# Kernel tuning notes

Hardware: AMD Instinct MI355X
Metric: run time of the kernel (lower is better)

The kernel has to match this reference:

```python
import jax, jax.numpy as jnp
import numpy as np

N, E, F, HID, HEADS, G = 20000, 320000, 64, 64, 4, 64
HC = HEADS * HID  # 256
NHID, NOUT = 256, 128
INV_SQRT2 = 0.7071067811865476


def _gat(x, src, dst, W, a_s, a_d, bias):
    # GATConv (v1), eval mode (no dropout); src/dst already include self-loops (PyG default)
    H, C = a_s.shape
    h = (x @ W).reshape(-1, H, C)  # [N,H,C]
    al_s = jnp.einsum('nhc,hc->nh', h, a_s)
    al_d = jnp.einsum('nhc,hc->nh', h, a_d)
    e = jax.nn.leaky_relu(al_s[src] + al_d[dst], 0.2)  # [Etot,H]
    m = jax.ops.segment_max(e, dst, num_segments=N)
    ex = jnp.exp(e - m[dst])
    den = jax.ops.segment_sum(ex, dst, num_segments=N)
    coef = ex / den[dst]  # softmax over incoming edges per target node
    out = jax.ops.segment_sum(h[src] * coef[:, :, None], dst, num_segments=N)
    return out.reshape(-1, H * C) + bias


def _bn(h, g, b):
    # BatchNorm1d, training-mode stats (biased var), eps=1e-5
    mu = h.mean(axis=0)
    var = h.var(axis=0)
    return g * (h - mu) * jax.lax.rsqrt(var + 1e-5) + b


def _block(x, src, dst, W1, a1s, a1d, b1, g1, be1, W2, a2s, a2d, b2, g2, be2, Wr, br, Wf, bf):
    h = jax.nn.relu(_bn(_gat(x, src, dst, W1, a1s, a1d, b1), g1, be1))
    h = jax.nn.relu(_bn(_gat(h, src, dst, W2, a2s, a2d, b2), g2, be2))
    res = x @ Wr + br
    return ((h + res) * INV_SQRT2) @ Wf + bf


def setup_inputs():
    ks = iter(jax.random.split(jax.random.key(0), 64))
    def rn(shape, scale=0.05):
        return jax.random.normal(next(ks), shape, dtype=jnp.float32) * scale
    inp = {}
    inp['x'] = jax.random.normal(next(ks), (N, F), dtype=jnp.float32)
    inp['edge_index'] = jax.random.randint(next(ks), (2, E), 0, N, dtype=jnp.int32)
    inp['batch'] = jnp.sort(jax.random.randint(next(ks), (N,), 0, G, dtype=jnp.int32))
    for b, cin in enumerate([F, HID]):
        p = 'b%d_' % b
        inp[p + 'W1'] = rn((cin, HC)); inp[p + 'a1s'] = rn((HEADS, HID)); inp[p + 'a1d'] = rn((HEADS, HID))
        inp[p + 'b1'] = jnp.zeros((HC,), jnp.float32)
        inp[p + 'g1'] = jnp.ones((HC,), jnp.float32); inp[p + 'be1'] = jnp.zeros((HC,), jnp.float32)
        inp[p + 'W2'] = rn((HC, HC)); inp[p + 'a2s'] = rn((1, HC)); inp[p + 'a2d'] = rn((1, HC))
        inp[p + 'b2'] = jnp.zeros((HC,), jnp.float32)
        inp[p + 'g2'] = jnp.ones((HC,), jnp.float32); inp[p + 'be2'] = jnp.zeros((HC,), jnp.float32)
        inp[p + 'Wr'] = rn((cin, HC)); inp[p + 'br'] = jnp.zeros((HC,), jnp.float32)
        inp[p + 'Wf'] = rn((HC, HID)); inp[p + 'bf'] = jnp.zeros((HID,), jnp.float32)
    inp['Wh1'] = rn((HID, NHID)); inp['bh1'] = jnp.zeros((NHID,), jnp.float32)
    inp['Wh2'] = rn((NHID, NOUT)); inp['bh2'] = jnp.zeros((NOUT,), jnp.float32)
    return inp


def reference(x, edge_index, batch,
              b0_W1, b0_a1s, b0_a1d, b0_b1, b0_g1, b0_be1, b0_W2, b0_a2s, b0_a2d, b0_b2, b0_g2, b0_be2, b0_Wr, b0_br, b0_Wf, b0_bf,
              b1_W1, b1_a1s, b1_a1d, b1_b1, b1_g1, b1_be1, b1_W2, b1_a2s, b1_a2d, b1_b2, b1_g2, b1_be2, b1_Wr, b1_br, b1_Wf, b1_bf,
              Wh1, bh1, Wh2, bh2):
    loops = jnp.arange(N, dtype=edge_index.dtype)
    src = jnp.concatenate([edge_index[0], loops])
    dst = jnp.concatenate([edge_index[1], loops])
    x = _block(x, src, dst, b0_W1, b0_a1s, b0_a1d, b0_b1, b0_g1, b0_be1, b0_W2, b0_a2s, b0_a2d, b0_b2, b0_g2, b0_be2, b0_Wr, b0_br, b0_Wf, b0_bf)
    x = _block(x, src, dst, b1_W1, b1_a1s, b1_a1d, b1_b1, b1_g1, b1_be1, b1_W2, b1_a2s, b1_a2d, b1_b2, b1_g2, b1_be2, b1_Wr, b1_br, b1_Wf, b1_bf)
    cnt = jax.ops.segment_sum(jnp.ones((N,), x.dtype), batch, num_segments=G)
    pooled = jax.ops.segment_sum(x, batch, num_segments=G) / jnp.maximum(cnt, 1.0)[:, None]
    h = jax.nn.relu(pooled @ Wh1 + bh1)
    return h @ Wh2 + bh2
```

## Files before the change

### kernel.cpp

```cpp
#include <hip/hip_runtime.h>

#define N_NODES 20000
#define N_EDGES 320000
#define ETOT (N_EDGES + N_NODES)
#define G_GROUPS 64

typedef __attribute__((ext_vector_type(8))) short bf16x8;
typedef __attribute__((ext_vector_type(4))) float f32x4;

__device__ __forceinline__ unsigned short f2bf(float f) {
    unsigned int u = __float_as_uint(f);
    u += 0x7fffu + ((u >> 16) & 1u);
    return (unsigned short)(u >> 16);
}
__device__ __forceinline__ float bf2f(unsigned short v) {
    return __uint_as_float(((unsigned int)v) << 16);
}
__device__ __forceinline__ unsigned int pack2bf(float a, float b) {
    return (unsigned int)f2bf(a) | ((unsigned int)f2bf(b) << 16);
}


__global__ __launch_bounds__(256) void k_hist(const int* __restrict__ ei, int* __restrict__ counts) {
    int e = blockIdx.x * 256 + threadIdx.x;
    if (e >= ETOT) return;
    int dst = (e < N_EDGES) ? ei[N_EDGES + e] : (e - N_EDGES);
    atomicAdd(&counts[dst], 1);
}

__global__ __launch_bounds__(1024) void k_scan(const int* __restrict__ counts, int* __restrict__ offs,
                                               int* __restrict__ cursor) {
    __shared__ int sdata[1024];
    const int t = threadIdx.x;
    const int chunk = (N_NODES + 1023) / 1024;
    int base = t * chunk;
    int s = 0;
    for (int i = 0; i < chunk; i++) { int idx = base + i; if (idx < N_NODES) s += counts[idx]; }
    sdata[t] = s;
    __syncthreads();
    for (int off = 1; off < 1024; off <<= 1) {
        int v = (t >= off) ? sdata[t - off] : 0;
        __syncthreads();
        sdata[t] += v;
        __syncthreads();
    }
    int prefix = (t == 0) ? 0 : sdata[t - 1];
    for (int i = 0; i < chunk; i++) {
        int idx = base + i;
        if (idx < N_NODES) {
            int cv = counts[idx];
            offs[idx] = prefix;
            cursor[idx] = prefix;
            prefix += cv;
        }
    }
    if (t == 1023) offs[N_NODES] = sdata[1023];
}

__global__ __launch_bounds__(256) void k_scatter(const int* __restrict__ ei, int* __restrict__ cursor,
                                                 int* __restrict__ csr_src) {
    int e = blockIdx.x * 256 + threadIdx.x;
    if (e >= ETOT) return;
    int src = (e < N_EDGES) ? ei[e] : (e - N_EDGES);
    int dst = (e < N_EDGES) ? ei[N_EDGES + e] : (e - N_EDGES);
    int p = atomicAdd(&cursor[dst], 1);
    csr_src[p] = src;
}


__global__ __launch_bounds__(256) void k_prepB(const float* __restrict__ W, unsigned short* __restrict__ Bf,
                                               int nfrag) {
    int s = blockIdx.x * 256 + threadIdx.x;
    if (s >= nfrag) return;
    int l = s & 63;
    int nt = (s >> 6) & 15;
    int kt = s >> 10;
    int n = nt * 16 + (l & 15);
    int kb = kt * 32 + (l >> 4) * 8;
    float v[8];
    #pragma unroll
    for (int j = 0; j < 8; j++) v[j] = W[(kb + j) * 256 + n];
    uint4 q = {pack2bf(v[0], v[1]), pack2bf(v[2], v[3]), pack2bf(v[4], v[5]), pack2bf(v[6], v[7])};
    *(uint4*)(Bf + s * 8) = q;
}


__global__ __launch_bounds__(256) void k_gemm64_dual(const float* __restrict__ x,
                                                     const unsigned short* __restrict__ Bf1,
                                                     const unsigned short* __restrict__ Bfr,
                                                     const float* __restrict__ br,
                                                     const float* __restrict__ a_s, const float* __restrict__ a_d,
                                                     unsigned short* __restrict__ hbf, float* __restrict__ res,
                                                     float* __restrict__ alS, float* __restrict__ alD) {
    const int rb = blockIdx.x >> 2, cs = blockIdx.x & 3;
    const int row0 = rb * 64;
    const int nrows = min(64, N_NODES - row0);
    const int t = threadIdx.x;
    const int w = t >> 6;
    const int l = t & 63;
    const int quad = l >> 4;
    const int colLocal = l & 15;
    __shared__ unsigned short As[8 * 64 * 8];
    __shared__ float alsm[4][64], aldm[4][64];

    const int ntg = cs * 4 + w;
    bf16x8 b1f[2], brf[2];
    #pragma unroll
    for (int kt = 0; kt < 2; kt++) {
        b1f[kt] = *(const bf16x8*)(Bf1 + ((kt * 16 + ntg) * 64 + l) * 8);
        brf[kt] = *(const bf16x8*)(Bfr + ((kt * 16 + ntg) * 64 + l) * 8);
    }

    #pragma unroll
    for (int gi = 0; gi < 2; gi++) {
        int g = 2 * w + gi;
        int kt = g >> 2, mt = g & 3;
        int sm = mt * 16 + (l & 15);
        int koff = kt * 32 + (l >> 4) * 8;
        float4 v0 = {0.f, 0.f, 0.f, 0.f}, v1 = {0.f, 0.f, 0.f, 0.f};
        if (sm < nrows) {
            v0 = *(const float4*)(x + (row0 + sm) * 64 + koff);
            v1 = *(const float4*)(x + (row0 + sm) * 64 + koff + 4);
        }
        uint4 q = {pack2bf(v0.x, v0.y), pack2bf(v0.z, v0.w), pack2bf(v1.x, v1.y), pack2bf(v1.z, v1.w)};
        *(uint4*)(As + (g * 64 + l) * 8) = q;
    }
    __syncthreads();

    f32x4 acc1[4], acc2[4];
    #pragma unroll
    for (int mt = 0; mt < 4; mt++) {
        acc1[mt] = (f32x4){0.f, 0.f, 0.f, 0.f};
        acc2[mt] = (f32x4){0.f, 0.f, 0.f, 0.f};
    }
    #pragma unroll
    for (int kt = 0; kt < 2; kt++) {
        #pragma unroll
        for (int mt = 0; mt < 4; mt++) {
            bf16x8 af = *(const bf16x8*)(As + ((kt * 4 + mt) * 64 + l) * 8);
            acc1[mt] = __builtin_amdgcn_mfma_f32_16x16x32_bf16(af, b1f[kt], acc1[mt], 0, 0, 0);
            acc2[mt] = __builtin_amdgcn_mfma_f32_16x16x32_bf16(af, brf[kt], acc2[mt], 0, 0, 0);
        }
    }

    const int col = cs * 64 + w * 16 + colLocal;
    const float brv = br[col];
    const float asv = a_s[col];
    const float adv = a_d[col];
    #pragma unroll
    for (int mt = 0; mt < 4; mt++) {
        #pragma unroll
        for (int r = 0; r < 4; r++) {
            float v1 = acc1[mt][r];
            int lr = mt * 16 + quad * 4 + r;
            bool ok = lr < nrows;
            int row = row0 + lr;
            if (ok) {
                hbf[row * 256 + col] = f2bf(v1);
                res[row * 256 + col] = acc2[mt][r] + brv;
            }
            float ps = v1 * asv, pd = v1 * adv;
            #pragma unroll
            for (int off = 1; off < 16; off <<= 1) {
                ps += __shfl_xor(ps, off);
                pd += __shfl_xor(pd, off);
            }
            if (colLocal == 0) {
                alsm[w][lr] = ps;
                aldm[w][lr] = pd;
            }
        }
    }
    __syncthreads();
    if (t < 64 && t < nrows) {
        float s = (alsm[0][t] + alsm[1][t]) + (alsm[2][t] + alsm[3][t]);
        float d = (aldm[0][t] + aldm[1][t]) + (aldm[2][t] + aldm[3][t]);
        alS[(row0 + t) * 4 + cs] = s;
        alD[(row0 + t) * 4 + cs] = d;
    }
}


template <int H>
__global__ __launch_bounds__(256) void k_agg(const unsigned short* __restrict__ hbf, const float* __restrict__ alS,
                                             const float* __restrict__ alD, const int* __restrict__ offs,
                                             const int* __restrict__ csr_src, const float* __restrict__ bias,
                                             float* __restrict__ out) {
    int node = blockIdx.x * 4 + (threadIdx.x >> 6);
    int lane = threadIdx.x & 63;
    if (node >= N_NODES) return;
    const int head = (H == 4) ? (lane >> 4) : 0;
    const float ald = alD[node * H + head];
    int e0 = offs[node], e1 = offs[node + 1];
    const unsigned short* hp = hbf + lane * 4;
    float den = 0.f, a0 = 0.f, a1 = 0.f, a2 = 0.f, a3 = 0.f;
    int e = e0;
    for (; e + 8 <= e1; e += 8) {
        int s[8];
        #pragma unroll
        for (int i = 0; i < 8; i++) s[i] = csr_src[e + i];
        ushort4 hq[8];
        #pragma unroll
        for (int i = 0; i < 8; i++) hq[i] = *(const ushort4*)(hp + s[i] * 256);
        float w[8];
        #pragma unroll
        for (int i = 0; i < 8; i++) {
            float v = alS[s[i] * H + head] + ald;
            v = (v > 0.f) ? v : 0.2f * v;
            w[i] = __expf(v);
        }
        #pragma unroll
        for (int i = 0; i < 8; i++) {
            den += w[i];
            a0 += w[i] * bf2f(hq[i].x); a1 += w[i] * bf2f(hq[i].y);
            a2 += w[i] * bf2f(hq[i].z); a3 += w[i] * bf2f(hq[i].w);
        }
    }
    for (; e < e1; e++) {
        int s = csr_src[e];
        float v = alS[s * H + head] + ald;
        v = (v > 0.f) ? v : 0.2f * v;
        float w = __expf(v);
        ushort4 hq = *(const ushort4*)(hp + s * 256);
        den += w;
        a0 += w * bf2f(hq.x); a1 += w * bf2f(hq.y); a2 += w * bf2f(hq.z); a3 += w * bf2f(hq.w);
    }
    float inv = 1.f / den;
    const float4 bv = *(const float4*)(bias + lane * 4);
    float4 o = {a0 * inv + bv.x, a1 * inv + bv.y, a2 * inv + bv.z, a3 * inv + bv.w};
    *(float4*)(out + node * 256 + lane * 4) = o;
}


__global__ __launch_bounds__(256) void k_bnstats_fin(const float* __restrict__ x, float* __restrict__ sum,
                                                     float* __restrict__ sumsq, const float* __restrict__ g,
                                                     const float* __restrict__ be, float* __restrict__ scale,
                                                     float* __restrict__ shift, int* __restrict__ counter) {
    const int c = threadIdx.x;
    float s = 0.f, q = 0.f;
    for (int r = blockIdx.x; r < N_NODES; r += gridDim.x) {
        float v = x[r * 256 + c];
        s += v; q += v * v;
    }
    atomicAdd(&sum[c], s);
    atomicAdd(&sumsq[c], q);
    __threadfence();
    __syncthreads();
    __shared__ int lastFlag;
    if (c == 0) lastFlag = (atomicAdd(counter, 1) == (int)gridDim.x - 1);
    __syncthreads();
    if (lastFlag) {
        float S = atomicAdd(&sum[c], 0.f);
        float Q = atomicAdd(&sumsq[c], 0.f);
        float mu = S * (1.f / N_NODES);
        float var = Q * (1.f / N_NODES) - mu * mu;
        float sc = g[c] * rsqrtf(var + 1e-5f);
        scale[c] = sc;
        shift[c] = be[c] - mu * sc;
        sum[c] = 0.f;
        sumsq[c] = 0.f;
        if (c == 0) *counter = 0;
    }
}


__global__ __launch_bounds__(256) void k_gemm256_mfma(const float* __restrict__ A, const float* __restrict__ scale,
                                                      const float* __restrict__ shift,
                                                      const unsigned short* __restrict__ Bf,
                                                      const float* __restrict__ a_s, const float* __restrict__ a_d,
                                                      unsigned short* __restrict__ C, float* __restrict__ alSp,
                                                      float* __restrict__ alDp) {
    const int rb = blockIdx.x >> 2, cs = blockIdx.x & 3;
    const int row0 = rb * 64;
    const int nrows = min(64, N_NODES - row0);
    const int t = threadIdx.x;
    const int w = t >> 6;
    const int l = t & 63;
    const int quad = l >> 4;
    const int colLocal = l & 15;
    __shared__ unsigned short As[2 * 4 * 64 * 8];
    __shared__ float scs[256], shs[256];
    scs[t] = scale[t];
    shs[t] = shift[t];

    const int ntg = cs * 4 + w;
    bf16x8 bfrag[8];
    #pragma unroll
    for (int kt = 0; kt < 8; kt++)
        bfrag[kt] = *(const bf16x8*)(Bf + ((kt * 16 + ntg) * 64 + l) * 8);

    f32x4 acc[4];
    #pragma unroll
    for (int mt = 0; mt < 4; mt++) acc[mt] = (f32x4){0.f, 0.f, 0.f, 0.f};

    const int smt = (t >> 6) & 3;
    const int sm = smt * 16 + (l & 15);
    const int skoff = (l >> 4) * 8;

    for (int kc = 0; kc < 4; kc++) {
        __syncthreads();
        #pragma unroll
        for (int kt2 = 0; kt2 < 2; kt2++) {
            int k = kc * 64 + kt2 * 32 + skoff;
            float4 v0 = {0.f, 0.f, 0.f, 0.f}, v1 = {0.f, 0.f, 0.f, 0.f};
            if (sm < nrows) {
                v0 = *(const float4*)(A + (row0 + sm) * 256 + k);
                v1 = *(const float4*)(A + (row0 + sm) * 256 + k + 4);
                v0.x = fmaxf(v0.x * scs[k + 0] + shs[k + 0], 0.f);
                v0.y = fmaxf(v0.y * scs[k + 1] + shs[k + 1], 0.f);
                v0.z = fmaxf(v0.z * scs[k + 2] + shs[k + 2], 0.f);
                v0.w = fmaxf(v0.w * scs[k + 3] + shs[k + 3], 0.f);
                v1.x = fmaxf(v1.x * scs[k + 4] + shs[k + 4], 0.f);
                v1.y = fmaxf(v1.y * scs[k + 5] + shs[k + 5], 0.f);
                v1.z = fmaxf(v1.z * scs[k + 6] + shs[k + 6], 0.f);
                v1.w = fmaxf(v1.w * scs[k + 7] + shs[k + 7], 0.f);
            }
            uint4 q = {pack2bf(v0.x, v0.y), pack2bf(v0.z, v0.w), pack2bf(v1.x, v1.y), pack2bf(v1.z, v1.w)};
            *(uint4*)(As + ((kt2 * 4 + smt) * 64 + l) * 8) = q;
        }
        __syncthreads();
        #pragma unroll
        for (int kt2 = 0; kt2 < 2; kt2++) {
            int ktg = kc * 2 + kt2;
            #pragma unroll
            for (int mt = 0; mt < 4; mt++) {
                bf16x8 af = *(const bf16x8*)(As + ((kt2 * 4 + mt) * 64 + l) * 8);
                acc[mt] = __builtin_amdgcn_mfma_f32_16x16x32_bf16(af, bfrag[ktg], acc[mt], 0, 0, 0);
            }
        }
    }

    const int col = cs * 64 + w * 16 + colLocal;
    const float asv = a_s[col];
    const float adv = a_d[col];
    #pragma unroll
    for (int mt = 0; mt < 4; mt++) {
        #pragma unroll
        for (int r = 0; r < 4; r++) {
            float v = acc[mt][r];
            int lr = mt * 16 + quad * 4 + r;
            bool ok = lr < nrows;
            int row = row0 + lr;
            if (ok) C[row * 256 + col] = f2bf(v);
            float ps = v * asv, pd = v * adv;
            #pragma unroll
            for (int off = 1; off < 16; off <<= 1) {
                ps += __shfl_xor(ps, off);
                pd += __shfl_xor(pd, off);
            }
            if (colLocal == 0 && ok) {
                alSp[ntg * N_NODES + row] = ps;
                alDp[ntg * N_NODES + row] = pd;
            }
        }
    }
}

__global__ __launch_bounds__(256) void k_alred(const float* __restrict__ alSp, const float* __restrict__ alDp,
                                               float* __restrict__ alS, float* __restrict__ alD) {
    int n = blockIdx.x * 256 + threadIdx.x;
    if (n >= N_NODES) return;
    float s = 0.f, d = 0.f;
    #pragma unroll
    for (int i = 0; i < 16; i++) {
        s += alSp[i * N_NODES + n];
        d += alDp[i * N_NODES + n];
    }
    alS[n] = s;
    alD[n] = d;
}


__global__ __launch_bounds__(256) void k_gemm_final(const float* __restrict__ A, const float* __restrict__ scale,
                                                    const float* __restrict__ shift, const float* __restrict__ res,
                                                    const float* __restrict__ B, const float* __restrict__ bias,
                                                    float* __restrict__ y) {
    const int row0 = blockIdx.x * 32;
    const int t = threadIdx.x;
    const float INVS = 0.70710678118654752440f;
    __shared__ float xs[32 * 36];
    __shared__ float bs[32 * 64];
    __shared__ float scs[256], shs[256];
    scs[t] = scale[t];
    shs[t] = shift[t];
    const int rf = (t & 15) | ((t >> 7) << 4);
    const int cf = (t >> 4) & 7;
    const int c0 = (t & 15) * 4;
    const int r0 = (t >> 4) * 2;
    float acc[2][4] = {};
    for (int k0 = 0; k0 < 256; k0 += 32) {
        __syncthreads();
        {
            int kcol = k0 + cf * 4;
            int gi = (row0 + rf) * 256 + kcol;
            float4 v = *(const float4*)(A + gi);
            float4 rv = *(const float4*)(res + gi);
            xs[(cf * 4 + 0) * 36 + rf] = (fmaxf(v.x * scs[kcol + 0] + shs[kcol + 0], 0.f) + rv.x) * INVS;
            xs[(cf * 4 + 1) * 36 + rf] = (fmaxf(v.y * scs[kcol + 1] + shs[kcol + 1], 0.f) + rv.y) * INVS;
            xs[(cf * 4 + 2) * 36 + rf] = (fmaxf(v.z * scs[kcol + 2] + shs[kcol + 2], 0.f) + rv.z) * INVS;
            xs[(cf * 4 + 3) * 36 + rf] = (fmaxf(v.w * scs[kcol + 3] + shs[kcol + 3], 0.f) + rv.w) * INVS;
        }
        {
            int cc = (t & 15) * 4;
            int k = t >> 4;
            #pragma unroll
            for (int pass = 0; pass < 2; pass++, k += 16) {
                *(float4*)(bs + k * 64 + cc) = *(const float4*)(B + (k0 + k) * 64 + cc);
            }
        }
        __syncthreads();
        #pragma unroll 8
        for (int k = 0; k < 32; k++) {
            float2 av = *(const float2*)(xs + k * 36 + r0);
            float4 bv = *(const float4*)(bs + k * 64 + c0);
            acc[0][0] += av.x * bv.x; acc[0][1] += av.x * bv.y;
            acc[0][2] += av.x * bv.z; acc[0][3] += av.x * bv.w;
            acc[1][0] += av.y * bv.x; acc[1][1] += av.y * bv.y;
            acc[1][2] += av.y * bv.z; acc[1][3] += av.y * bv.w;
        }
    }
    float4 bv = *(const float4*)(bias + c0);
    #pragma unroll
    for (int i = 0; i < 2; i++) {
        int gr = row0 + r0 + i;
        float4 o = {acc[i][0] + bv.x, acc[i][1] + bv.y, acc[i][2] + bv.z, acc[i][3] + bv.w};
        *(float4*)(y + gr * 64 + c0) = o;
    }
}


__global__ __launch_bounds__(256) void k_pool_head(const float* __restrict__ x, const int* __restrict__ batch,
                                                   const float* __restrict__ Wh1, const float* __restrict__ bh1,
                                                   const float* __restrict__ Wh2, const float* __restrict__ bh2,
                                                   float* __restrict__ out) {
    const int g = blockIdx.x;
    const int t = threadIdx.x;
    int lo = 0, hi = N_NODES;
    while (lo < hi) { int mid = (lo + hi) >> 1; if (batch[mid] < g) lo = mid + 1; else hi = mid; }
    int start = lo;
    hi = N_NODES;
    while (lo < hi) { int mid = (lo + hi) >> 1; if (batch[mid] < g + 1) lo = mid + 1; else hi = mid; }
    int end = lo;
    float cnt = (float)(end - start);

    __shared__ float part[256];
    __shared__ float p[64];
    __shared__ float hrow[256];
    const int c = t & 63;
    float s = 0.f;
    for (int r = start + (t >> 6); r < end; r += 4) s += x[r * 64 + c];
    part[t] = s;
    __syncthreads();
    if (t < 64) {
        float v = part[t] + part[t + 64] + part[t + 128] + part[t + 192];
        p[t] = v / fmaxf(cnt, 1.f);
    }
    __syncthreads();
    float a = bh1[t];
    #pragma unroll 8
    for (int k = 0; k < 64; k++) a += p[k] * Wh1[k * 256 + t];
    hrow[t] = fmaxf(a, 0.f);
    __syncthreads();
    if (t < 128) {
        float o = bh2[t];
        #pragma unroll 8
        for (int k = 0; k < 256; k++) o += hrow[k] * Wh2[k * 128 + t];
        out[g * 128 + t] = o;
    }
}


extern "C" void kernel_launch(void* const* d_in, const int* in_sizes, int n_in,
                              void* d_out, int out_size, void* d_ws, size_t ws_size,
                              hipStream_t stream) {
    (void)in_sizes; (void)n_in; (void)out_size; (void)ws_size;
    const float* x0 = (const float*)d_in[0];
    const int* ei = (const int*)d_in[1];
    const int* batch = (const int*)d_in[2];
    const float* Wh1 = (const float*)d_in[35];
    const float* bh1 = (const float*)d_in[36];
    const float* Wh2 = (const float*)d_in[37];
    const float* bh2 = (const float*)d_in[38];

    char* p = (char*)d_ws;
    auto alloc = [&](size_t bytes) -> void* {
        void* r = (void*)p;
        p += (bytes + 255) & ~(size_t)255;
        return r;
    };
    int* counts = (int*)alloc((size_t)N_NODES * 4);
    float* bnsum = (float*)alloc(2048);
    float* bnsq = bnsum + 256;
    int* bncnt = (int*)alloc(256);
    const size_t zero_bytes = (((size_t)N_NODES * 4 + 255) & ~(size_t)255) + 2048 + 256;
    int* offs = (int*)alloc((size_t)(N_NODES + 1) * 4);
    int* cursor = (int*)alloc((size_t)N_NODES * 4);
    int* csr_src = (int*)alloc((size_t)ETOT * 4);
    float* alS = (float*)alloc((size_t)N_NODES * 4 * 4);
    float* alD = (float*)alloc((size_t)N_NODES * 4 * 4);
    float* alSp = (float*)alloc((size_t)N_NODES * 16 * 4);
    float* alDp = (float*)alloc((size_t)N_NODES * 16 * 4);
    float* scaleb = (float*)alloc(1024);
    float* shiftb = (float*)alloc(1024);
    unsigned short* hbuf = (unsigned short*)alloc((size_t)N_NODES * 256 * 2);
    float* obuf = (float*)alloc((size_t)N_NODES * 256 * 4);
    float* rbuf = (float*)alloc((size_t)N_NODES * 256 * 4);
    float* xout = (float*)alloc((size_t)N_NODES * 64 * 4);
    unsigned short* Bf2_0 = (unsigned short*)alloc(256 * 256 * 2);
    unsigned short* Bf2_1 = (unsigned short*)alloc(256 * 256 * 2);
    unsigned short* Bf1_0 = (unsigned short*)alloc(64 * 256 * 2);
    unsigned short* Bfr_0 = (unsigned short*)alloc(64 * 256 * 2);
    unsigned short* Bf1_1 = (unsigned short*)alloc(64 * 256 * 2);
    unsigned short* Bfr_1 = (unsigned short*)alloc(64 * 256 * 2);

    hipMemsetAsync(counts, 0, zero_bytes, stream);
    k_hist<<<(ETOT + 255) / 256, 256, 0, stream>>>(ei, counts);
    k_scan<<<1, 1024, 0, stream>>>(counts, offs, cursor);
    k_scatter<<<(ETOT + 255) / 256, 256, 0, stream>>>(ei, cursor, csr_src);
    k_prepB<<<32, 256, 0, stream>>>((const float*)d_in[3 + 6], Bf2_0, 8192);
    k_prepB<<<32, 256, 0, stream>>>((const float*)d_in[19 + 6], Bf2_1, 8192);
    k_prepB<<<8, 256, 0, stream>>>((const float*)d_in[3 + 0], Bf1_0, 2048);
    k_prepB<<<8, 256, 0, stream>>>((const float*)d_in[3 + 12], Bfr_0, 2048);
    k_prepB<<<8, 256, 0, stream>>>((const float*)d_in[19 + 0], Bf1_1, 2048);
    k_prepB<<<8, 256, 0, stream>>>((const float*)d_in[19 + 12], Bfr_1, 2048);

    const int tile64_blocks = ((N_NODES + 63) / 64) * 4;
    const int node_blocks = (N_NODES + 3) / 4;
    const int red_blocks = (N_NODES + 255) / 256;
    const int final_blocks = N_NODES / 32;

    auto run_block = [&](const float* xin, int base, const unsigned short* Bf2,
                         const unsigned short* Bf1, const unsigned short* Bfr) {
        const float* a1s = (const float*)d_in[base + 1];
        const float* a1d = (const float*)d_in[base + 2];
        const float* b1 = (const float*)d_in[base + 3];
        const float* g1 = (const float*)d_in[base + 4];
        const float* be1 = (const float*)d_in[base + 5];
        const float* a2s = (const float*)d_in[base + 7];
        const float* a2d = (const float*)d_in[base + 8];
        const float* b2 = (const float*)d_in[base + 9];
        const float* g2 = (const float*)d_in[base + 10];
        const float* be2 = (const float*)d_in[base + 11];
        const float* br = (const float*)d_in[base + 13];
        const float* Wf = (const float*)d_in[base + 14];
        const float* bf = (const float*)d_in[base + 15];

        k_gemm64_dual<<<tile64_blocks, 256, 0, stream>>>(xin, Bf1, Bfr, br, a1s, a1d, hbuf, rbuf, alS, alD);
        k_agg<4><<<node_blocks, 256, 0, stream>>>(hbuf, alS, alD, offs, csr_src, b1, obuf);
        k_bnstats_fin<<<256, 256, 0, stream>>>(obuf, bnsum, bnsq, g1, be1, scaleb, shiftb, bncnt);
        k_gemm256_mfma<<<tile64_blocks, 256, 0, stream>>>(obuf, scaleb, shiftb, Bf2, a2s, a2d, hbuf, alSp, alDp);
        k_alred<<<red_blocks, 256, 0, stream>>>(alSp, alDp, alS, alD);
        k_agg<1><<<node_blocks, 256, 0, stream>>>(hbuf, alS, alD, offs, csr_src, b2, obuf);
        k_bnstats_fin<<<256, 256, 0, stream>>>(obuf, bnsum, bnsq, g2, be2, scaleb, shiftb, bncnt);
        k_gemm_final<<<final_blocks, 256, 0, stream>>>(obuf, scaleb, shiftb, rbuf, Wf, bf, xout);
    };

    run_block(x0, 3, Bf2_0, Bf1_0, Bfr_0);
    run_block(xout, 19, Bf2_1, Bf1_1, Bfr_1);

    k_pool_head<<<G_GROUPS, 256, 0, stream>>>(xout, batch, Wh1, bh1, Wh2, bh2, (float*)d_out);
}
```

Baseline: 634.1 us.

## Fuse weight prep launches, replace alpha partial reduction with atomics, vectorize agg loads

Merges the six weight-conversion launches into one kernel. Removes the separate partial-sum reduction kernel for attention logits in the second GAT layer: the GEMM now atomically accumulates into zeroed per-node buffers, and the zeroing is folded into the preceding BN stats kernel. In the aggregation kernel, the node index is made wave-uniform and the 4-head logits are read as a float4. This trades a launch and a 16-way partial buffer for float atomics, which makes the logit sums order-nondeterministic.

```diff
diff --git a/kernel.cpp b/kernel.cpp
--- a/kernel.cpp
+++ b/kernel.cpp
@@ -68,10 +68,23 @@
 }
 
 
-__global__ __launch_bounds__(256) void k_prepB(const float* __restrict__ W, unsigned short* __restrict__ Bf,
-                                               int nfrag) {
-    int s = blockIdx.x * 256 + threadIdx.x;
-    if (s >= nfrag) return;
+__global__ __launch_bounds__(256) void k_prepB_all(const float* __restrict__ W2a, const float* __restrict__ W2b,
+                                                   const float* __restrict__ W1a, const float* __restrict__ Wra,
+                                                   const float* __restrict__ W1b, const float* __restrict__ Wrb,
+                                                   unsigned short* __restrict__ B2a, unsigned short* __restrict__ B2b,
+                                                   unsigned short* __restrict__ B1a, unsigned short* __restrict__ Bra,
+                                                   unsigned short* __restrict__ B1b, unsigned short* __restrict__ Brb) {
+    int b = blockIdx.x;
+    const float* W;
+    unsigned short* Bf;
+    int s0;
+    if (b < 32) { W = W2a; Bf = B2a; s0 = b; }
+    else if (b < 64) { W = W2b; Bf = B2b; s0 = b - 32; }
+    else if (b < 72) { W = W1a; Bf = B1a; s0 = b - 64; }
+    else if (b < 80) { W = Wra; Bf = Bra; s0 = b - 72; }
+    else if (b < 88) { W = W1b; Bf = B1b; s0 = b - 80; }
+    else { W = Wrb; Bf = Brb; s0 = b - 88; }
+    int s = s0 * 256 + threadIdx.x;
     int l = s & 63;
     int nt = (s >> 6) & 15;
     int kt = s >> 10;
@@ -186,12 +199,17 @@
                                              const float* __restrict__ alD, const int* __restrict__ offs,
                                              const int* __restrict__ csr_src, const float* __restrict__ bias,
                                              float* __restrict__ out) {
-    int node = blockIdx.x * 4 + (threadIdx.x >> 6);
-    int lane = threadIdx.x & 63;
-    if (node >= N_NODES) return;
+    const int node = __builtin_amdgcn_readfirstlane(blockIdx.x * 4 + (threadIdx.x >> 6));
+    const int lane = threadIdx.x & 63;
     const int head = (H == 4) ? (lane >> 4) : 0;
-    const float ald = alD[node * H + head];
-    int e0 = offs[node], e1 = offs[node + 1];
+    float ald;
+    if (H == 4) {
+        float4 d4 = *(const float4*)(alD + node * 4);
+        ald = (head == 0) ? d4.x : (head == 1) ? d4.y : (head == 2) ? d4.z : d4.w;
+    } else {
+        ald = alD[node];
+    }
+    const int e0 = offs[node], e1 = offs[node + 1];
     const unsigned short* hp = hbf + lane * 4;
     float den = 0.f, a0 = 0.f, a1 = 0.f, a2 = 0.f, a3 = 0.f;
     int e = e0;
@@ -205,7 +223,14 @@
         float w[8];
         #pragma unroll
         for (int i = 0; i < 8; i++) {
-            float v = alS[s[i] * H + head] + ald;
+            float v;
+            if (H == 4) {
+                float4 s4 = *(const float4*)(alS + s[i] * 4);
+                float as = (head == 0) ? s4.x : (head == 1) ? s4.y : (head == 2) ? s4.z : s4.w;
+                v = as + ald;
+            } else {
+                v = alS[s[i]] + ald;
+            }
             v = (v > 0.f) ? v : 0.2f * v;
             w[i] = __expf(v);
         }
@@ -218,7 +243,14 @@
     }
     for (; e < e1; e++) {
         int s = csr_src[e];
-        float v = alS[s * H + head] + ald;
+        float v;
+        if (H == 4) {
+            float4 s4 = *(const float4*)(alS + s * 4);
+            float as = (head == 0) ? s4.x : (head == 1) ? s4.y : (head == 2) ? s4.z : s4.w;
+            v = as + ald;
+        } else {
+            v = alS[s] + ald;
+        }
         v = (v > 0.f) ? v : 0.2f * v;
         float w = __expf(v);
         ushort4 hq = *(const ushort4*)(hp + s * 256);
@@ -235,8 +267,13 @@
 __global__ __launch_bounds__(256) void k_bnstats_fin(const float* __restrict__ x, float* __restrict__ sum,
                                                      float* __restrict__ sumsq, const float* __restrict__ g,
                                                      const float* __restrict__ be, float* __restrict__ scale,
-                                                     float* __restrict__ shift, int* __restrict__ counter) {
+                                                     float* __restrict__ shift, int* __restrict__ counter,
+                                                     float* __restrict__ zS, float* __restrict__ zD) {
     const int c = threadIdx.x;
+    if (zS) {
+        int idx = blockIdx.x * 256 + c;
+        if (idx < N_NODES) { zS[idx] = 0.f; zD[idx] = 0.f; }
+    }
     float s = 0.f, q = 0.f;
     for (int r = blockIdx.x; r < N_NODES; r += gridDim.x) {
         float v = x[r * 256 + c];
@@ -268,8 +305,8 @@
                                                       const float* __restrict__ shift,
                                                       const unsigned short* __restrict__ Bf,
                                                       const float* __restrict__ a_s, const float* __restrict__ a_d,
-                                                      unsigned short* __restrict__ C, float* __restrict__ alSp,
-                                                      float* __restrict__ alDp) {
+                                                      unsigned short* __restrict__ C, float* __restrict__ alS2,
+                                                      float* __restrict__ alD2) {
     const int rb = blockIdx.x >> 2, cs = blockIdx.x & 3;
     const int row0 = rb * 64;
     const int nrows = min(64, N_NODES - row0);
@@ -349,25 +386,11 @@
                 pd += __shfl_xor(pd, off);
             }
             if (colLocal == 0 && ok) {
-                alSp[ntg * N_NODES + row] = ps;
-                alDp[ntg * N_NODES + row] = pd;
-            }
-        }
-    }
-}
-
-__global__ __launch_bounds__(256) void k_alred(const float* __restrict__ alSp, const float* __restrict__ alDp,
-                                               float* __restrict__ alS, float* __restrict__ alD) {
-    int n = blockIdx.x * 256 + threadIdx.x;
-    if (n >= N_NODES) return;
-    float s = 0.f, d = 0.f;
-    #pragma unroll
-    for (int i = 0; i < 16; i++) {
-        s += alSp[i * N_NODES + n];
-        d += alDp[i * N_NODES + n];
-    }
-    alS[n] = s;
-    alD[n] = d;
+                atomicAdd(&alS2[row], ps);
+                atomicAdd(&alD2[row], pd);
+            }
+        }
+    }
 }
 
 
@@ -498,8 +521,8 @@
     int* csr_src = (int*)alloc((size_t)ETOT * 4);
     float* alS = (float*)alloc((size_t)N_NODES * 4 * 4);
     float* alD = (float*)alloc((size_t)N_NODES * 4 * 4);
-    float* alSp = (float*)alloc((size_t)N_NODES * 16 * 4);
-    float* alDp = (float*)alloc((size_t)N_NODES * 16 * 4);
+    float* alS2 = (float*)alloc((size_t)N_NODES * 4);
+    float* alD2 = (float*)alloc((size_t)N_NODES * 4);
     float* scaleb = (float*)alloc(1024);
     float* shiftb = (float*)alloc(1024);
     unsigned short* hbuf = (unsigned short*)alloc((size_t)N_NODES * 256 * 2);
@@ -517,16 +540,13 @@
     k_hist<<<(ETOT + 255) / 256, 256, 0, stream>>>(ei, counts);
     k_scan<<<1, 1024, 0, stream>>>(counts, offs, cursor);
     k_scatter<<<(ETOT + 255) / 256, 256, 0, stream>>>(ei, cursor, csr_src);
-    k_prepB<<<32, 256, 0, stream>>>((const float*)d_in[3 + 6], Bf2_0, 8192);
-    k_prepB<<<32, 256, 0, stream>>>((const float*)d_in[19 + 6], Bf2_1, 8192);
-    k_prepB<<<8, 256, 0, stream>>>((const float*)d_in[3 + 0], Bf1_0, 2048);
-    k_prepB<<<8, 256, 0, stream>>>((const float*)d_in[3 + 12], Bfr_0, 2048);
-    k_prepB<<<8, 256, 0, stream>>>((const float*)d_in[19 + 0], Bf1_1, 2048);
-    k_prepB<<<8, 256, 0, stream>>>((const float*)d_in[19 + 12], Bfr_1, 2048);
+    k_prepB_all<<<96, 256, 0, stream>>>((const float*)d_in[3 + 6], (const float*)d_in[19 + 6],
+                                        (const float*)d_in[3 + 0], (const float*)d_in[3 + 12],
+                                        (const float*)d_in[19 + 0], (const float*)d_in[19 + 12],
+                                        Bf2_0, Bf2_1, Bf1_0, Bfr_0, Bf1_1, Bfr_1);
 
     const int tile64_blocks = ((N_NODES + 63) / 64) * 4;
-    const int node_blocks = (N_NODES + 3) / 4;
-    const int red_blocks = (N_NODES + 255) / 256;
+    const int node_blocks = N_NODES / 4;
     const int final_blocks = N_NODES / 32;
 
     auto run_block = [&](const float* xin, int base, const unsigned short* Bf2,
@@ -547,11 +567,10 @@
 
         k_gemm64_dual<<<tile64_blocks, 256, 0, stream>>>(xin, Bf1, Bfr, br, a1s, a1d, hbuf, rbuf, alS, alD);
         k_agg<4><<<node_blocks, 256, 0, stream>>>(hbuf, alS, alD, offs, csr_src, b1, obuf);
-        k_bnstats_fin<<<256, 256, 0, stream>>>(obuf, bnsum, bnsq, g1, be1, scaleb, shiftb, bncnt);
-        k_gemm256_mfma<<<tile64_blocks, 256, 0, stream>>>(obuf, scaleb, shiftb, Bf2, a2s, a2d, hbuf, alSp, alDp);
-        k_alred<<<red_blocks, 256, 0, stream>>>(alSp, alDp, alS, alD);
-        k_agg<1><<<node_blocks, 256, 0, stream>>>(hbuf, alS, alD, offs, csr_src, b2, obuf);
-        k_bnstats_fin<<<256, 256, 0, stream>>>(obuf, bnsum, bnsq, g2, be2, scaleb, shiftb, bncnt);
+        k_bnstats_fin<<<256, 256, 0, stream>>>(obuf, bnsum, bnsq, g1, be1, scaleb, shiftb, bncnt, alS2, alD2);
+        k_gemm256_mfma<<<tile64_blocks, 256, 0, stream>>>(obuf, scaleb, shiftb, Bf2, a2s, a2d, hbuf, alS2, alD2);
+        k_agg<1><<<node_blocks, 256, 0, stream>>>(hbuf, alS2, alD2, offs, csr_src, b2, obuf);
+        k_bnstats_fin<<<256, 256, 0, stream>>>(obuf, bnsum, bnsq, g2, be2, scaleb, shiftb, bncnt, nullptr, nullptr);
         k_gemm_final<<<final_blocks, 256, 0, stream>>>(obuf, scaleb, shiftb, rbuf, Wf, bf, xout);
     };
 
```

New measurement: 626.9 us. Within noise of the previous version (-1.1%).
